# Performance work log

Hardware: AMD Instinct MI355X
Metric: run time of the kernel (lower is better)

Reference implementation:

```python
import jax, jax.numpy as jnp
import numpy as np

B, H, T, N, DK = 4, 8, 12, 325, 32


def setup_inputs() -> dict:
    key = jax.random.key(0)
    ks = jax.random.split(key, 8)
    shp = (B, H, T, N, DK)
    return {
        "Qf": jax.random.normal(ks[0], shp, jnp.float32),
        "Kf": jax.random.normal(ks[1], shp, jnp.float32),
        "Vf": jax.random.normal(ks[2], shp, jnp.float32),
        "Qs": jax.random.normal(ks[3], shp, jnp.float32),
        "Ks": jax.random.normal(ks[4], shp, jnp.float32),
        "Vs": jax.random.normal(ks[5], shp, jnp.float32),
        "Kj": jax.random.normal(ks[6], (N, 1), jnp.float32),   # FlowSpeed jam density param
        "Vf_p": jax.random.normal(ks[7], (N, 1), jnp.float32),  # FlowSpeed free-flow speed param
    }


def reference(Qf, Kf, Vf, Qs, Ks, Vs, Kj, Vf_p):
    d_k = Qf.shape[-1]
    scale = 1.0 / np.sqrt(d_k).astype(np.float32)

    # FlowSpeed nonlinearity: flow = Kj * (speed - speed^2 / (Vf + 1e-5))
    # Kj, Vf_p: (N,1) broadcast over (..., N, d_k)
    Qf_from_speed = Kj * (Qs - jnp.square(Qs) / (Vf_p + 1e-5))

    def attn(q, k, v):
        # q,k,v: [B,H,T,N,dk]; scores: [B,H,T,N,N]
        scores = jnp.einsum("bhtnd,bhtmd->bhtnm", q, k) * scale
        return jnp.einsum("bhtnm,bhtmd->bhtnd", jax.nn.softmax(scores, axis=-1), v)

    context_flow_flow = attn(Qf, Kf, Vf)
    context_flow_speed = attn(Kf, Qf_from_speed, Vf)
    context_speed_flow = attn(Ks, Qf, Vs)
    context_speed_speed = attn(Qs, Ks, Vs)
    return (context_flow_flow, context_flow_speed, context_speed_flow, context_speed_speed)
```

## Files before the change

kernel.cpp:

```cpp
#include <hip/hip_runtime.h>
#include <hip/hip_bf16.h>

typedef float f32x4 __attribute__((ext_vector_type(4)));
typedef short short8 __attribute__((ext_vector_type(8)));

#define NT    325
#define DKK   32
#define NSL   384
#define SLICE (NT*DKK)
#define TOTE  (NSL*SLICE)
#define NKT   21
#define PADV  352
#define VGRAN (32 * (PADV/8))
#define PP    40
#define SCALE2 0.25506372f

__device__ __forceinline__ int swz(int sidx, int row) { return sidx ^ ((row & 7) << 3); }

__device__ __forceinline__ unsigned cvtpk(float lo, float hi) {
    unsigned r;
    asm("v_cvt_pk_bf16_f32 %0, %1, %2" : "=v"(r) : "v"(lo), "v"(hi));
    return r;
}
__device__ __forceinline__ unsigned pk2_split(float x, float y, unsigned& lopk) {
    const unsigned hi = cvtpk(x, y);
    const float hx = __builtin_bit_cast(float, hi << 16);
    const float hy = __builtin_bit_cast(float, hi & 0xffff0000u);
    lopk = cvtpk(x - hx, y - hy);
    return hi;
}

__global__ __launch_bounds__(512, 4)
void attn4_mfma(const float* __restrict__ Qf, const float* __restrict__ Kf,
                const float* __restrict__ Vf, const float* __restrict__ Qs,
                const float* __restrict__ Ks, const float* __restrict__ Vs,
                const float* __restrict__ Kj, const float* __restrict__ Vfp,
                float* __restrict__ out)
{
    __shared__ __align__(16) unsigned short Kb[336 * DKK];
    __shared__ __align__(16) unsigned short Kl[336 * DKK];
    __shared__ __align__(16) unsigned short Vt[DKK * PADV];
    __shared__ __align__(16) unsigned short Pl[8][16 * PP];

    const int tid = threadIdx.x;
    const int bid = blockIdx.x;
    const int g8  = bid >> 3, xx = bid & 7;
    const int var = (xx + g8) & 3;
    const int bt  = 2 * g8 + (xx >> 2);
    const size_t base = (size_t)bt * SLICE;

    const float *qp, *kp, *vp;
    if      (var == 0) { qp = Qf; kp = Kf; vp = Vf; }
    else if (var == 1) { qp = Kf; kp = Qs; vp = Vf; }
    else if (var == 2) { qp = Ks; kp = Qf; vp = Vs; }
    else               { qp = Qs; kp = Ks; vp = Vs; }
    float* op = out + (size_t)var * TOTE + base;

    for (int i8 = tid; i8 < SLICE / 8; i8 += 512) {
        const int idx = i8 * 8;
        const int m   = idx >> 5;
        const int sidx = swz(idx, m);
        const float* s = kp + base + idx;
        float4 a = *(const float4*)s;
        float4 b = *(const float4*)(s + 4);
        if (var == 1) {
            const float kj = Kj[m];
            const float rv = 1.0f / (Vfp[m] + 1e-5f);
            a.x = kj * (a.x - a.x * a.x * rv);
            a.y = kj * (a.y - a.y * a.y * rv);
            a.z = kj * (a.z - a.z * a.z * rv);
            a.w = kj * (a.w - a.w * a.w * rv);
            b.x = kj * (b.x - b.x * b.x * rv);
            b.y = kj * (b.y - b.y * b.y * rv);
            b.z = kj * (b.z - b.z * b.z * rv);
            b.w = kj * (b.w - b.w * b.w * rv);
            uint4 hw, lw;
            hw.x = pk2_split(a.x, a.y, lw.x);
            hw.y = pk2_split(a.z, a.w, lw.y);
            hw.z = pk2_split(b.x, b.y, lw.z);
            hw.w = pk2_split(b.z, b.w, lw.w);
            *(uint4*)&Kb[sidx] = hw;
            *(uint4*)&Kl[sidx] = lw;
        } else {
            uint4 pkv;
            pkv.x = cvtpk(a.x, a.y); pkv.y = cvtpk(a.z, a.w);
            pkv.z = cvtpk(b.x, b.y); pkv.w = cvtpk(b.z, b.w);
            *(uint4*)&Kb[sidx] = pkv;
        }
    }

    for (int gi = tid; gi < VGRAN; gi += 512) {
        const int dd = gi / 44;
        const int m8 = gi - dd * 44;
        const int mb = m8 * 8;
        float v[8];
        #pragma unroll
        for (int i = 0; i < 8; ++i) {
            const int m = mb + i;
            v[i] = (m < NT) ? vp[base + (size_t)m * DKK + dd] : 0.0f;
        }
        uint4 pkv;
        pkv.x = cvtpk(v[0], v[1]); pkv.y = cvtpk(v[2], v[3]);
        pkv.z = cvtpk(v[4], v[5]); pkv.w = cvtpk(v[6], v[7]);
        *(uint4*)&Vt[swz(dd * PADV + mb, dd)] = pkv;
    }
    __syncthreads();

    const int lane = tid & 63;
    const int wv   = tid >> 6;
    const int c    = lane & 15;
    const int g    = lane >> 4;
    const int kswz = (c & 7) << 3;
    const f32x4 zero = {0.f, 0.f, 0.f, 0.f};
    unsigned short* const pw = &Pl[wv][0];

    int qt = wv;
    float4 qa, qb;
    {
        int qr = qt * 16 + c; if (qr > NT - 1) qr = NT - 1;
        const float* s = qp + base + (size_t)qr * DKK + g * 8;
        qa = *(const float4*)s; qb = *(const float4*)(s + 4);
    }

    for (; qt < NKT; qt += 8) {
        float4 na, nb;
        const bool more = (qt + 8) < NKT;
        if (more) {
            int qr = (qt + 8) * 16 + c; if (qr > NT - 1) qr = NT - 1;
            const float* s = qp + base + (size_t)qr * DKK + g * 8;
            na = *(const float4*)s; nb = *(const float4*)(s + 4);
        }

        uint4 qwh, qwl;
        qwh.x = pk2_split(qa.x * SCALE2, qa.y * SCALE2, qwl.x);
        qwh.y = pk2_split(qa.z * SCALE2, qa.w * SCALE2, qwl.y);
        qwh.z = pk2_split(qb.x * SCALE2, qb.y * SCALE2, qwl.z);
        qwh.w = pk2_split(qb.z * SCALE2, qb.w * SCALE2, qwl.w);
        const short8 qh = __builtin_bit_cast(short8, qwh);
        const short8 ql = __builtin_bit_cast(short8, qwl);

        f32x4 o0 = zero, o1 = zero;
        float ts = 0.f;
        float mrow = -1e30f;

        #pragma unroll
        for (int ks = 0; ks < 11; ++ks) {
            const int fi0 = (((2 * ks) * 16 + c) * DKK + g * 8) ^ kswz;
            const int fi1 = fi0 + 16 * DKK;
            f32x4 a0, a1;

            __builtin_amdgcn_s_setprio(1);
            if (var != 1) {
                const short8 k0 = *(const short8*)&Kb[fi0];
                a0 = __builtin_amdgcn_mfma_f32_16x16x32_bf16(k0, qh, zero, 0, 0, 0);
                if (ks < 10) {
                    const short8 k1 = *(const short8*)&Kb[fi1];
                    a1 = __builtin_amdgcn_mfma_f32_16x16x32_bf16(k1, qh, zero, 0, 0, 0);
                }
            } else {
                {
                    const short8 kh = *(const short8*)&Kb[fi0];
                    const short8 kl = *(const short8*)&Kl[fi0];
                    f32x4 t = __builtin_amdgcn_mfma_f32_16x16x32_bf16(kh, ql, zero, 0, 0, 0);
                    t = __builtin_amdgcn_mfma_f32_16x16x32_bf16(kl, qh, t, 0, 0, 0);
                    a0 = __builtin_amdgcn_mfma_f32_16x16x32_bf16(kh, qh, t, 0, 0, 0);
                }
                if (ks < 10) {
                    const short8 kh = *(const short8*)&Kb[fi1];
                    const short8 kl = *(const short8*)&Kl[fi1];
                    f32x4 t = __builtin_amdgcn_mfma_f32_16x16x32_bf16(kh, ql, zero, 0, 0, 0);
                    t = __builtin_amdgcn_mfma_f32_16x16x32_bf16(kl, qh, t, 0, 0, 0);
                    a1 = __builtin_amdgcn_mfma_f32_16x16x32_bf16(kh, qh, t, 0, 0, 0);
                }
            }
            __builtin_amdgcn_s_setprio(0);

            if (ks == 10) {
                #pragma unroll
                for (int r = 0; r < 4; ++r)
                    a0[r] = (4 * g + r > 4) ? -1e30f : a0[r];
            }

            if (var == 1) {
                float pm = fmaxf(fmaxf(a0[0], a0[1]), fmaxf(a0[2], a0[3]));
                if (ks < 10)
                    pm = fmaxf(pm, fmaxf(fmaxf(a1[0], a1[1]), fmaxf(a1[2], a1[3])));
                pm = fmaxf(pm, __shfl_xor(pm, 16));
                pm = fmaxf(pm, __shfl_xor(pm, 32));
                if (__any(pm > mrow)) {
                    const float mnew = fmaxf(mrow, pm);
                    const float f = exp2f(mrow - mnew);
                    mrow = mnew;
                    ts *= f;
                    #pragma unroll
                    for (int r = 0; r < 4; ++r) {
                        const float fr = __shfl(f, 4 * g + r);
                        o0[r] *= fr; o1[r] *= fr;
                    }
                }
                #pragma unroll
                for (int r = 0; r < 4; ++r) { a0[r] = exp2f(a0[r] - mrow); ts += a0[r]; }
                if (ks < 10) {
                    #pragma unroll
                    for (int r = 0; r < 4; ++r) { a1[r] = exp2f(a1[r] - mrow); ts += a1[r]; }
                }
            } else {
                #pragma unroll
                for (int r = 0; r < 4; ++r) { a0[r] = exp2f(a0[r]); ts += a0[r]; }
                if (ks < 10) {
                    #pragma unroll
                    for (int r = 0; r < 4; ++r) { a1[r] = exp2f(a1[r]); ts += a1[r]; }
                }
            }

            {
                uint2 wa; wa.x = cvtpk(a0[0], a0[1]); wa.y = cvtpk(a0[2], a0[3]);
                *(uint2*)&pw[c * PP + 4 * g] = wa;
                uint2 wb;
                if (ks < 10) { wb.x = cvtpk(a1[0], a1[1]); wb.y = cvtpk(a1[2], a1[3]); }
                else         { wb.x = 0u; wb.y = 0u; }
                *(uint2*)&pw[c * PP + 16 + 4 * g] = wb;
            }
            const short8 af = *(const short8*)&pw[c * PP + 8 * g];
            const short8 v0 = *(const short8*)&Vt[( c        * PADV + ks * 32 + g * 8) ^ kswz];
            const short8 v1 = *(const short8*)&Vt[((c + 16)  * PADV + ks * 32 + g * 8) ^ kswz];
            __builtin_amdgcn_s_setprio(1);
            o0 = __builtin_amdgcn_mfma_f32_16x16x32_bf16(af, v0, o0, 0, 0, 0);
            o1 = __builtin_amdgcn_mfma_f32_16x16x32_bf16(af, v1, o1, 0, 0, 0);
            __builtin_amdgcn_s_setprio(0);
        }

        ts += __shfl_xor(ts, 16);
        ts += __shfl_xor(ts, 32);
        const float inv = 1.0f / ts;

        #pragma unroll
        for (int r = 0; r < 4; ++r) {
            const int row = qt * 16 + 4 * g + r;
            const float iv = __shfl(inv, 4 * g + r);
            if (row < NT) {
                op[(size_t)row * DKK + c]      = o0[r] * iv;
                op[(size_t)row * DKK + c + 16] = o1[r] * iv;
            }
        }
        qa = na; qb = nb;
    }
}

extern "C" void kernel_launch(void* const* d_in, const int* in_sizes, int n_in,
                              void* d_out, int out_size, void* d_ws, size_t ws_size,
                              hipStream_t stream) {
    const float* Qf  = (const float*)d_in[0];
    const float* Kf  = (const float*)d_in[1];
    const float* Vf  = (const float*)d_in[2];
    const float* Qs  = (const float*)d_in[3];
    const float* Ks  = (const float*)d_in[4];
    const float* Vs  = (const float*)d_in[5];
    const float* Kj  = (const float*)d_in[6];
    const float* Vfp = (const float*)d_in[7];
    float* out = (float*)d_out;

    attn4_mfma<<<dim3(NSL * 4), dim3(512), 0, stream>>>(Qf, Kf, Vf, Qs, Ks, Vs, Kj, Vfp, out);
}
```

Measured before the change: 121.1 us.

## Process two query tiles per wave and repack P in registers via permlane swaps

Each wave now handles two query tiles at once in its first pass, so every K fragment loaded from LDS feeds MFMAs for both tiles. The LDS round trip that transposed the softmax probabilities into MFMA A-operand layout is replaced by in-register repacking with v_permlane32/16_swap instructions, and the per-wave P scratch buffer is removed. The variant branch becomes a template parameter, so the split-precision path and the plain path compile separately. This raises register pressure, which could reduce occupancy at 512 threads and 4 blocks per SM, and it depends on the permlane lane mapping being correct.

```diff
diff --git a/kernel.cpp b/kernel.cpp
--- a/kernel.cpp
+++ b/kernel.cpp
@@ -12,7 +12,6 @@
 #define NKT   21
 #define PADV  352
 #define VGRAN (32 * (PADV/8))
-#define PP    40
 #define SCALE2 0.25506372f
 
 __device__ __forceinline__ int swz(int sidx, int row) { return sidx ^ ((row & 7) << 3); }
@@ -28,6 +27,238 @@
     const float hy = __builtin_bit_cast(float, hi & 0xffff0000u);
     lopk = cvtpk(x - hx, y - hy);
     return hi;
+}
+__device__ __forceinline__ void swap32(unsigned& a, unsigned& b) {
+    asm("v_permlane32_swap_b32 %0, %1" : "+v"(a), "+v"(b));
+}
+__device__ __forceinline__ void swap16(unsigned& a, unsigned& b) {
+    asm("v_permlane16_swap_b32 %0, %1" : "+v"(a), "+v"(b));
+}
+
+__device__ __forceinline__ short8 repack(const f32x4& a0, const f32x4& a1, bool hasB) {
+    unsigned u = cvtpk(a0[0], a0[1]);
+    unsigned v = cvtpk(a0[2], a0[3]);
+    unsigned s = hasB ? cvtpk(a1[0], a1[1]) : 0u;
+    unsigned t = hasB ? cvtpk(a1[2], a1[3]) : 0u;
+    swap32(u, s); swap16(u, s);
+    swap32(v, t); swap16(v, t);
+    uint4 w; w.x = u; w.y = v; w.z = s; w.w = t;
+    return __builtin_bit_cast(short8, w);
+}
+
+template <bool SPLIT>
+__device__ __forceinline__ void load_q(const float* qsrc, short8& qh, short8& ql) {
+    const float4 qa = *(const float4*)qsrc;
+    const float4 qb = *(const float4*)(qsrc + 4);
+    uint4 h, l;
+    if constexpr (SPLIT) {
+        h.x = pk2_split(qa.x * SCALE2, qa.y * SCALE2, l.x);
+        h.y = pk2_split(qa.z * SCALE2, qa.w * SCALE2, l.y);
+        h.z = pk2_split(qb.x * SCALE2, qb.y * SCALE2, l.z);
+        h.w = pk2_split(qb.z * SCALE2, qb.w * SCALE2, l.w);
+        ql = __builtin_bit_cast(short8, l);
+    } else {
+        h.x = cvtpk(qa.x * SCALE2, qa.y * SCALE2);
+        h.y = cvtpk(qa.z * SCALE2, qa.w * SCALE2);
+        h.z = cvtpk(qb.x * SCALE2, qb.y * SCALE2);
+        h.w = cvtpk(qb.z * SCALE2, qb.w * SCALE2);
+    }
+    qh = __builtin_bit_cast(short8, h);
+}
+
+template <bool SPLIT>
+__device__ __forceinline__ void process(
+    const float* __restrict__ qp, size_t base, float* __restrict__ op,
+    const unsigned short* Kb, const unsigned short* Kl, const unsigned short* Vt,
+    int c, int g, int wv, int kswz)
+{
+    const f32x4 zero = {0.f, 0.f, 0.f, 0.f};
+
+    for (int pass = 0; pass < 2; ++pass) {
+        if (pass == 1 && wv >= NKT - 16) return;
+        const bool dual = (pass == 0);
+        const int qtA = dual ? wv : 16 + wv;
+        const int qtB = wv + 8;
+
+        short8 qhA, qlA, qhB, qlB;
+        {
+            int qr = qtA * 16 + c; if (qr > NT - 1) qr = NT - 1;
+            load_q<SPLIT>(qp + base + (size_t)qr * DKK + g * 8, qhA, qlA);
+        }
+        if (dual) {
+            const int qr = qtB * 16 + c;
+            load_q<SPLIT>(qp + base + (size_t)qr * DKK + g * 8, qhB, qlB);
+        }
+
+        f32x4 oA0 = zero, oA1 = zero, oB0 = zero, oB1 = zero;
+        float tsA = 0.f, tsB = 0.f, mA = -1e30f, mB = -1e30f;
+
+        #pragma unroll
+        for (int ks = 0; ks < 11; ++ks) {
+            const int fi0 = (((2 * ks) * 16 + c) * DKK + g * 8) ^ kswz;
+            const int fi1 = fi0 + 16 * DKK;
+            const bool hasB1 = (ks < 10);
+            f32x4 aA0, aA1, aB0, aB1;
+
+            __builtin_amdgcn_s_setprio(1);
+            if constexpr (SPLIT) {
+                const short8 kh0 = *(const short8*)&Kb[fi0];
+                const short8 kl0 = *(const short8*)&Kl[fi0];
+                { f32x4 t = __builtin_amdgcn_mfma_f32_16x16x32_bf16(kh0, qlA, zero, 0, 0, 0);
+                  t = __builtin_amdgcn_mfma_f32_16x16x32_bf16(kl0, qhA, t, 0, 0, 0);
+                  aA0 = __builtin_amdgcn_mfma_f32_16x16x32_bf16(kh0, qhA, t, 0, 0, 0); }
+                if (dual) {
+                  f32x4 t = __builtin_amdgcn_mfma_f32_16x16x32_bf16(kh0, qlB, zero, 0, 0, 0);
+                  t = __builtin_amdgcn_mfma_f32_16x16x32_bf16(kl0, qhB, t, 0, 0, 0);
+                  aB0 = __builtin_amdgcn_mfma_f32_16x16x32_bf16(kh0, qhB, t, 0, 0, 0); }
+                if (hasB1) {
+                    const short8 kh1 = *(const short8*)&Kb[fi1];
+                    const short8 kl1 = *(const short8*)&Kl[fi1];
+                    { f32x4 t = __builtin_amdgcn_mfma_f32_16x16x32_bf16(kh1, qlA, zero, 0, 0, 0);
+                      t = __builtin_amdgcn_mfma_f32_16x16x32_bf16(kl1, qhA, t, 0, 0, 0);
+                      aA1 = __builtin_amdgcn_mfma_f32_16x16x32_bf16(kh1, qhA, t, 0, 0, 0); }
+                    if (dual) {
+                      f32x4 t = __builtin_amdgcn_mfma_f32_16x16x32_bf16(kh1, qlB, zero, 0, 0, 0);
+                      t = __builtin_amdgcn_mfma_f32_16x16x32_bf16(kl1, qhB, t, 0, 0, 0);
+                      aB1 = __builtin_amdgcn_mfma_f32_16x16x32_bf16(kh1, qhB, t, 0, 0, 0); }
+                }
+            } else {
+                const short8 k0 = *(const short8*)&Kb[fi0];
+                aA0 = __builtin_amdgcn_mfma_f32_16x16x32_bf16(k0, qhA, zero, 0, 0, 0);
+                if (dual) aB0 = __builtin_amdgcn_mfma_f32_16x16x32_bf16(k0, qhB, zero, 0, 0, 0);
+                if (hasB1) {
+                    const short8 k1 = *(const short8*)&Kb[fi1];
+                    aA1 = __builtin_amdgcn_mfma_f32_16x16x32_bf16(k1, qhA, zero, 0, 0, 0);
+                    if (dual) aB1 = __builtin_amdgcn_mfma_f32_16x16x32_bf16(k1, qhB, zero, 0, 0, 0);
+                }
+            }
+            __builtin_amdgcn_s_setprio(0);
+
+            if (ks == 10) {
+                #pragma unroll
+                for (int r = 0; r < 4; ++r) {
+                    aA0[r] = (4 * g + r > 4) ? -1e30f : aA0[r];
+                    if (dual) aB0[r] = (4 * g + r > 4) ? -1e30f : aB0[r];
+                }
+            }
+
+            if constexpr (SPLIT) {
+                {
+                    float pm = fmaxf(fmaxf(aA0[0], aA0[1]), fmaxf(aA0[2], aA0[3]));
+                    if (hasB1) pm = fmaxf(pm, fmaxf(fmaxf(aA1[0], aA1[1]), fmaxf(aA1[2], aA1[3])));
+                    pm = fmaxf(pm, __shfl_xor(pm, 16));
+                    pm = fmaxf(pm, __shfl_xor(pm, 32));
+                    if (__any(pm > mA)) {
+                        const float mn = fmaxf(mA, pm);
+                        const float f = exp2f(mA - mn);
+                        mA = mn; tsA *= f;
+                        #pragma unroll
+                        for (int r = 0; r < 4; ++r) {
+                            const float fr = __shfl(f, 4 * g + r);
+                            oA0[r] *= fr; oA1[r] *= fr;
+                        }
+                    }
+                    #pragma unroll
+                    for (int r = 0; r < 4; ++r) aA0[r] = exp2f(aA0[r] - mA);
+                    tsA += (aA0[0] + aA0[1]) + (aA0[2] + aA0[3]);
+                    if (hasB1) {
+                        #pragma unroll
+                        for (int r = 0; r < 4; ++r) aA1[r] = exp2f(aA1[r] - mA);
+                        tsA += (aA1[0] + aA1[1]) + (aA1[2] + aA1[3]);
+                    }
+                }
+                if (dual) {
+                    float pm = fmaxf(fmaxf(aB0[0], aB0[1]), fmaxf(aB0[2], aB0[3]));
+                    if (hasB1) pm = fmaxf(pm, fmaxf(fmaxf(aB1[0], aB1[1]), fmaxf(aB1[2], aB1[3])));
+                    pm = fmaxf(pm, __shfl_xor(pm, 16));
+                    pm = fmaxf(pm, __shfl_xor(pm, 32));
+                    if (__any(pm > mB)) {
+                        const float mn = fmaxf(mB, pm);
+                        const float f = exp2f(mB - mn);
+                        mB = mn; tsB *= f;
+                        #pragma unroll
+                        for (int r = 0; r < 4; ++r) {
+                            const float fr = __shfl(f, 4 * g + r);
+                            oB0[r] *= fr; oB1[r] *= fr;
+                        }
+                    }
+                    #pragma unroll
+                    for (int r = 0; r < 4; ++r) aB0[r] = exp2f(aB0[r] - mB);
+                    tsB += (aB0[0] + aB0[1]) + (aB0[2] + aB0[3]);
+                    if (hasB1) {
+                        #pragma unroll
+                        for (int r = 0; r < 4; ++r) aB1[r] = exp2f(aB1[r] - mB);
+                        tsB += (aB1[0] + aB1[1]) + (aB1[2] + aB1[3]);
+                    }
+                }
+            } else {
+                #pragma unroll
+                for (int r = 0; r < 4; ++r) aA0[r] = exp2f(aA0[r]);
+                tsA += (aA0[0] + aA0[1]) + (aA0[2] + aA0[3]);
+                if (hasB1) {
+                    #pragma unroll
+                    for (int r = 0; r < 4; ++r) aA1[r] = exp2f(aA1[r]);
+                    tsA += (aA1[0] + aA1[1]) + (aA1[2] + aA1[3]);
+                }
+                if (dual) {
+                    #pragma unroll
+                    for (int r = 0; r < 4; ++r) aB0[r] = exp2f(aB0[r]);
+                    tsB += (aB0[0] + aB0[1]) + (aB0[2] + aB0[3]);
+                    if (hasB1) {
+                        #pragma unroll
+                        for (int r = 0; r < 4; ++r) aB1[r] = exp2f(aB1[r]);
+                        tsB += (aB1[0] + aB1[1]) + (aB1[2] + aB1[3]);
+                    }
+                }
+            }
+
+            const short8 v0 = *(const short8*)&Vt[( c        * PADV + ks * 32 + g * 8) ^ kswz];
+            const short8 v1 = *(const short8*)&Vt[((c + 16)  * PADV + ks * 32 + g * 8) ^ kswz];
+            {
+                const short8 af = repack(aA0, hasB1 ? aA1 : aA0, hasB1);
+                __builtin_amdgcn_s_setprio(1);
+                oA0 = __builtin_amdgcn_mfma_f32_16x16x32_bf16(af, v0, oA0, 0, 0, 0);
+                oA1 = __builtin_amdgcn_mfma_f32_16x16x32_bf16(af, v1, oA1, 0, 0, 0);
+                __builtin_amdgcn_s_setprio(0);
+            }
+            if (dual) {
+                const short8 af = repack(aB0, hasB1 ? aB1 : aB0, hasB1);
+                __builtin_amdgcn_s_setprio(1);
+                oB0 = __builtin_amdgcn_mfma_f32_16x16x32_bf16(af, v0, oB0, 0, 0, 0);
+                oB1 = __builtin_amdgcn_mfma_f32_16x16x32_bf16(af, v1, oB1, 0, 0, 0);
+                __builtin_amdgcn_s_setprio(0);
+            }
+        }
+
+        {
+            float ts = tsA;
+            ts += __shfl_xor(ts, 16);
+            ts += __shfl_xor(ts, 32);
+            const float inv = 1.0f / ts;
+            #pragma unroll
+            for (int r = 0; r < 4; ++r) {
+                const int row = qtA * 16 + 4 * g + r;
+                const float iv = __shfl(inv, 4 * g + r);
+                if (row < NT) {
+                    op[(size_t)row * DKK + c]      = oA0[r] * iv;
+                    op[(size_t)row * DKK + c + 16] = oA1[r] * iv;
+                }
+            }
+        }
+        if (dual) {
+            float ts = tsB;
+            ts += __shfl_xor(ts, 16);
+            ts += __shfl_xor(ts, 32);
+            const float inv = 1.0f / ts;
+            #pragma unroll
+            for (int r = 0; r < 4; ++r) {
+                const int row = qtB * 16 + 4 * g + r;
+                const float iv = __shfl(inv, 4 * g + r);
+                op[(size_t)row * DKK + c]      = oB0[r] * iv;
+                op[(size_t)row * DKK + c + 16] = oB1[r] * iv;
+            }
+        }
+    }
 }
 
 __global__ __launch_bounds__(512, 4)
@@ -40,7 +271,6 @@
     __shared__ __align__(16) unsigned short Kb[336 * DKK];
     __shared__ __align__(16) unsigned short Kl[336 * DKK];
     __shared__ __align__(16) unsigned short Vt[DKK * PADV];
-    __shared__ __align__(16) unsigned short Pl[8][16 * PP];
 
     const int tid = threadIdx.x;
     const int bid = blockIdx.x;
@@ -111,140 +341,9 @@
     const int c    = lane & 15;
     const int g    = lane >> 4;
     const int kswz = (c & 7) << 3;
-    const f32x4 zero = {0.f, 0.f, 0.f, 0.f};
-    unsigned short* const pw = &Pl[wv][0];
-
-    int qt = wv;
-    float4 qa, qb;
-    {
-        int qr = qt * 16 + c; if (qr > NT - 1) qr = NT - 1;
-        const float* s = qp + base + (size_t)qr * DKK + g * 8;
-        qa = *(const float4*)s; qb = *(const float4*)(s + 4);
-    }
-
-    for (; qt < NKT; qt += 8) {
-        float4 na, nb;
-        const bool more = (qt + 8) < NKT;
-        if (more) {
-            int qr = (qt + 8) * 16 + c; if (qr > NT - 1) qr = NT - 1;
-            const float* s = qp + base + (size_t)qr * DKK + g * 8;
-            na = *(const float4*)s; nb = *(const float4*)(s + 4);
-        }
-
-        uint4 qwh, qwl;
-        qwh.x = pk2_split(qa.x * SCALE2, qa.y * SCALE2, qwl.x);
-        qwh.y = pk2_split(qa.z * SCALE2, qa.w * SCALE2, qwl.y);
-        qwh.z = pk2_split(qb.x * SCALE2, qb.y * SCALE2, qwl.z);
-        qwh.w = pk2_split(qb.z * SCALE2, qb.w * SCALE2, qwl.w);
-        const short8 qh = __builtin_bit_cast(short8, qwh);
-        const short8 ql = __builtin_bit_cast(short8, qwl);
-
-        f32x4 o0 = zero, o1 = zero;
-        float ts = 0.f;
-        float mrow = -1e30f;
-
-        #pragma unroll
-        for (int ks = 0; ks < 11; ++ks) {
-            const int fi0 = (((2 * ks) * 16 + c) * DKK + g * 8) ^ kswz;
-            const int fi1 = fi0 + 16 * DKK;
-            f32x4 a0, a1;
-
-            __builtin_amdgcn_s_setprio(1);
-            if (var != 1) {
-                const short8 k0 = *(const short8*)&Kb[fi0];
-                a0 = __builtin_amdgcn_mfma_f32_16x16x32_bf16(k0, qh, zero, 0, 0, 0);
-                if (ks < 10) {
-                    const short8 k1 = *(const short8*)&Kb[fi1];
-                    a1 = __builtin_amdgcn_mfma_f32_16x16x32_bf16(k1, qh, zero, 0, 0, 0);
-                }
-            } else {
-                {
-                    const short8 kh = *(const short8*)&Kb[fi0];
-                    const short8 kl = *(const short8*)&Kl[fi0];
-                    f32x4 t = __builtin_amdgcn_mfma_f32_16x16x32_bf16(kh, ql, zero, 0, 0, 0);
-                    t = __builtin_amdgcn_mfma_f32_16x16x32_bf16(kl, qh, t, 0, 0, 0);
-                    a0 = __builtin_amdgcn_mfma_f32_16x16x32_bf16(kh, qh, t, 0, 0, 0);
-                }
-                if (ks < 10) {
-                    const short8 kh = *(const short8*)&Kb[fi1];
-                    const short8 kl = *(const short8*)&Kl[fi1];
-                    f32x4 t = __builtin_amdgcn_mfma_f32_16x16x32_bf16(kh, ql, zero, 0, 0, 0);
-                    t = __builtin_amdgcn_mfma_f32_16x16x32_bf16(kl, qh, t, 0, 0, 0);
-                    a1 = __builtin_amdgcn_mfma_f32_16x16x32_bf16(kh, qh, t, 0, 0, 0);
-                }
-            }
-            __builtin_amdgcn_s_setprio(0);
-
-            if (ks == 10) {
-                #pragma unroll
-                for (int r = 0; r < 4; ++r)
-                    a0[r] = (4 * g + r > 4) ? -1e30f : a0[r];
-            }
-
-            if (var == 1) {
-                float pm = fmaxf(fmaxf(a0[0], a0[1]), fmaxf(a0[2], a0[3]));
-                if (ks < 10)
-                    pm = fmaxf(pm, fmaxf(fmaxf(a1[0], a1[1]), fmaxf(a1[2], a1[3])));
-                pm = fmaxf(pm, __shfl_xor(pm, 16));
-                pm = fmaxf(pm, __shfl_xor(pm, 32));
-                if (__any(pm > mrow)) {
-                    const float mnew = fmaxf(mrow, pm);
-                    const float f = exp2f(mrow - mnew);
-                    mrow = mnew;
-                    ts *= f;
-                    #pragma unroll
-                    for (int r = 0; r < 4; ++r) {
-                        const float fr = __shfl(f, 4 * g + r);
-                        o0[r] *= fr; o1[r] *= fr;
-                    }
-                }
-                #pragma unroll
-                for (int r = 0; r < 4; ++r) { a0[r] = exp2f(a0[r] - mrow); ts += a0[r]; }
-                if (ks < 10) {
-                    #pragma unroll
-                    for (int r = 0; r < 4; ++r) { a1[r] = exp2f(a1[r] - mrow); ts += a1[r]; }
-                }
-            } else {
-                #pragma unroll
-                for (int r = 0; r < 4; ++r) { a0[r] = exp2f(a0[r]); ts += a0[r]; }
-                if (ks < 10) {
-                    #pragma unroll
-                    for (int r = 0; r < 4; ++r) { a1[r] = exp2f(a1[r]); ts += a1[r]; }
-                }
-            }
-
-            {
-                uint2 wa; wa.x = cvtpk(a0[0], a0[1]); wa.y = cvtpk(a0[2], a0[3]);
-                *(uint2*)&pw[c * PP + 4 * g] = wa;
-                uint2 wb;
-                if (ks < 10) { wb.x = cvtpk(a1[0], a1[1]); wb.y = cvtpk(a1[2], a1[3]); }
-                else         { wb.x = 0u; wb.y = 0u; }
-                *(uint2*)&pw[c * PP + 16 + 4 * g] = wb;
-            }
-            const short8 af = *(const short8*)&pw[c * PP + 8 * g];
-            const short8 v0 = *(const short8*)&Vt[( c        * PADV + ks * 32 + g * 8) ^ kswz];
-            const short8 v1 = *(const short8*)&Vt[((c + 16)  * PADV + ks * 32 + g * 8) ^ kswz];
-            __builtin_amdgcn_s_setprio(1);
-            o0 = __builtin_amdgcn_mfma_f32_16x16x32_bf16(af, v0, o0, 0, 0, 0);
-            o1 = __builtin_amdgcn_mfma_f32_16x16x32_bf16(af, v1, o1, 0, 0, 0);
-            __builtin_amdgcn_s_setprio(0);
-        }
-
-        ts += __shfl_xor(ts, 16);
-        ts += __shfl_xor(ts, 32);
-        const float inv = 1.0f / ts;
-
-        #pragma unroll
-        for (int r = 0; r < 4; ++r) {
-            const int row = qt * 16 + 4 * g + r;
-            const float iv = __shfl(inv, 4 * g + r);
-            if (row < NT) {
-                op[(size_t)row * DKK + c]      = o0[r] * iv;
-                op[(size_t)row * DKK + c + 16] = o1[r] * iv;
-            }
-        }
-        qa = na; qb = nb;
-    }
+
+    if (var == 1) process<true >(qp, base, op, Kb, Kl, Vt, c, g, wv, kswz);
+    else          process<false>(qp, base, op, Kb, Kl, Vt, c, g, wv, kswz);
 }
 
 extern "C" void kernel_launch(void* const* d_in, const int* in_sizes, int n_in,
```

After: 140.5 us. 1.16x slower.

## Drop low-part K LDS buffer; recompute bf16 residual from global in loop

Applied to the files above, without the earlier changes.

Removes the Kl shared-memory array that held the low bf16 half of the transformed K for the FlowSpeed variant. Instead, each lane rereads the fp32 source from global memory inside the score loop and recomputes the residual against the high part already in LDS. This cuts LDS use, likely so more blocks fit per CU, but the launch-bounds minimum occupancy is lowered from 4 to 3. In exchange, the var==1 path gains global loads, a reciprocal and extra ALU work per tile, and the setprio calls now wrap only the non-FlowSpeed branch.

```diff
diff --git a/kernel.cpp b/kernel.cpp
--- a/kernel.cpp
+++ b/kernel.cpp
@@ -30,7 +30,24 @@
     return hi;
 }
 
-__global__ __launch_bounds__(512, 4)
+__device__ __forceinline__ short8 make_kl(const float* qsrc, float kj, float rv, short8 kh) {
+    const float4 qa = *(const float4*)qsrc;
+    const float4 qb = *(const float4*)(qsrc + 4);
+    const float q[8] = {qa.x, qa.y, qa.z, qa.w, qb.x, qb.y, qb.z, qb.w};
+    float d[8];
+    #pragma unroll
+    for (int i = 0; i < 8; ++i) {
+        const float kv = kj * (q[i] - q[i] * q[i] * rv);
+        const unsigned hb = ((unsigned)(unsigned short)kh[i]) << 16;
+        d[i] = kv - __builtin_bit_cast(float, hb);
+    }
+    uint4 l;
+    l.x = cvtpk(d[0], d[1]); l.y = cvtpk(d[2], d[3]);
+    l.z = cvtpk(d[4], d[5]); l.w = cvtpk(d[6], d[7]);
+    return __builtin_bit_cast(short8, l);
+}
+
+__global__ __launch_bounds__(512, 3)
 void attn4_mfma(const float* __restrict__ Qf, const float* __restrict__ Kf,
                 const float* __restrict__ Vf, const float* __restrict__ Qs,
                 const float* __restrict__ Ks, const float* __restrict__ Vs,
@@ -38,7 +55,6 @@
                 float* __restrict__ out)
 {
     __shared__ __align__(16) unsigned short Kb[336 * DKK];
-    __shared__ __align__(16) unsigned short Kl[336 * DKK];
     __shared__ __align__(16) unsigned short Vt[DKK * PADV];
     __shared__ __align__(16) unsigned short Pl[8][16 * PP];
 
@@ -74,19 +90,11 @@
             b.y = kj * (b.y - b.y * b.y * rv);
             b.z = kj * (b.z - b.z * b.z * rv);
             b.w = kj * (b.w - b.w * b.w * rv);
-            uint4 hw, lw;
-            hw.x = pk2_split(a.x, a.y, lw.x);
-            hw.y = pk2_split(a.z, a.w, lw.y);
-            hw.z = pk2_split(b.x, b.y, lw.z);
-            hw.w = pk2_split(b.z, b.w, lw.w);
-            *(uint4*)&Kb[sidx] = hw;
-            *(uint4*)&Kl[sidx] = lw;
-        } else {
-            uint4 pkv;
-            pkv.x = cvtpk(a.x, a.y); pkv.y = cvtpk(a.z, a.w);
-            pkv.z = cvtpk(b.x, b.y); pkv.w = cvtpk(b.z, b.w);
-            *(uint4*)&Kb[sidx] = pkv;
-        }
+        }
+        uint4 pkv;
+        pkv.x = cvtpk(a.x, a.y); pkv.y = cvtpk(a.z, a.w);
+        pkv.z = cvtpk(b.x, b.y); pkv.w = cvtpk(b.z, b.w);
+        *(uint4*)&Kb[sidx] = pkv;
     }
 
     for (int gi = tid; gi < VGRAN; gi += 512) {
@@ -149,31 +157,38 @@
             const int fi1 = fi0 + 16 * DKK;
             f32x4 a0, a1;
 
-            __builtin_amdgcn_s_setprio(1);
             if (var != 1) {
+                __builtin_amdgcn_s_setprio(1);
                 const short8 k0 = *(const short8*)&Kb[fi0];
                 a0 = __builtin_amdgcn_mfma_f32_16x16x32_bf16(k0, qh, zero, 0, 0, 0);
                 if (ks < 10) {
                     const short8 k1 = *(const short8*)&Kb[fi1];
                     a1 = __builtin_amdgcn_mfma_f32_16x16x32_bf16(k1, qh, zero, 0, 0, 0);
                 }
+                __builtin_amdgcn_s_setprio(0);
             } else {
+                const int row0 = (2 * ks) * 16 + c;
+                const int r0 = row0 < NT ? row0 : NT - 1;
+                const float kj0 = Kj[r0];
+                const float rv0 = 1.0f / (Vfp[r0] + 1e-5f);
+                const short8 kh0 = *(const short8*)&Kb[fi0];
+                const short8 kl0 = make_kl(kp + base + (size_t)r0 * DKK + g * 8, kj0, rv0, kh0);
                 {
-                    const short8 kh = *(const short8*)&Kb[fi0];
-                    const short8 kl = *(const short8*)&Kl[fi0];
-                    f32x4 t = __builtin_amdgcn_mfma_f32_16x16x32_bf16(kh, ql, zero, 0, 0, 0);
-                    t = __builtin_amdgcn_mfma_f32_16x16x32_bf16(kl, qh, t, 0, 0, 0);
-                    a0 = __builtin_amdgcn_mfma_f32_16x16x32_bf16(kh, qh, t, 0, 0, 0);
-                }
-                if (ks < 10) {
-                    const short8 kh = *(const short8*)&Kb[fi1];
-                    const short8 kl = *(const short8*)&Kl[fi1];
-                    f32x4 t = __builtin_amdgcn_mfma_f32_16x16x32_bf16(kh, ql, zero, 0, 0, 0);
-                    t = __builtin_amdgcn_mfma_f32_16x16x32_bf16(kl, qh, t, 0, 0, 0);
-                    a1 = __builtin_amdgcn_mfma_f32_16x16x32_bf16(kh, qh, t, 0, 0, 0);
-                }
-            }
-            __builtin_amdgcn_s_setprio(0);
+                    f32x4 t = __builtin_amdgcn_mfma_f32_16x16x32_bf16(kh0, ql, zero, 0, 0, 0);
+                    t = __builtin_amdgcn_mfma_f32_16x16x32_bf16(kl0, qh, t, 0, 0, 0);
+                    a0 = __builtin_amdgcn_mfma_f32_16x16x32_bf16(kh0, qh, t, 0, 0, 0);
+                }
+                if (ks < 10) {
+                    const int r1 = row0 + 16;
+                    const float kj1 = Kj[r1];
+                    const float rv1 = 1.0f / (Vfp[r1] + 1e-5f);
+                    const short8 kh1 = *(const short8*)&Kb[fi1];
+                    const short8 kl1 = make_kl(kp + base + (size_t)r1 * DKK + g * 8, kj1, rv1, kh1);
+                    f32x4 t = __builtin_amdgcn_mfma_f32_16x16x32_bf16(kh1, ql, zero, 0, 0, 0);
+                    t = __builtin_amdgcn_mfma_f32_16x16x32_bf16(kl1, qh, t, 0, 0, 0);
+                    a1 = __builtin_amdgcn_mfma_f32_16x16x32_bf16(kh1, qh, t, 0, 0, 0);
+                }
+            }
 
             if (ks == 10) {
                 #pragma unroll
@@ -188,10 +203,9 @@
                 pm = fmaxf(pm, __shfl_xor(pm, 16));
                 pm = fmaxf(pm, __shfl_xor(pm, 32));
                 if (__any(pm > mrow)) {
-                    const float mnew = fmaxf(mrow, pm);
-                    const float f = exp2f(mrow - mnew);
-                    mrow = mnew;
-                    ts *= f;
+                    const float mn = fmaxf(mrow, pm);
+                    const float f = exp2f(mrow - mn);
+                    mrow = mn; ts *= f;
                     #pragma unroll
                     for (int r = 0; r < 4; ++r) {
                         const float fr = __shfl(f, 4 * g + r);
```

New measurement: 296.3 us. 2.45x slower.
